# Kernel tuning notes

Measured on AMD Instinct MI355X. Metric: run time of the kernel, lower is better.

The kernel has to match this reference:

```python
import jax, jax.numpy as jnp
import numpy as np

N_NODES = 50000
N_EDGES = 800000
N_GRAPHS = 512
HEADS = 4
HDIM = 64
NEG_SLOPE = 0.2


def setup_inputs() -> dict:
    key = jax.random.key(0)
    ks = jax.random.split(key, 16)
    x = jax.random.normal(ks[0], (N_NODES, 128), dtype=jnp.float32)
    edge_index = jax.random.randint(ks[1], (2, N_EDGES), 0, N_NODES, dtype=jnp.int64)
    batch = jnp.sort(jax.random.randint(ks[2], (N_NODES,), 0, N_GRAPHS, dtype=jnp.int64))
    def glorot(k, shape):
        fan = shape[0] + shape[-1]
        return jax.random.normal(k, shape, dtype=jnp.float32) * jnp.sqrt(2.0 / fan)
    return {
        "x": x, "edge_index": edge_index, "batch": batch,
        "W1": glorot(ks[3], (128, 256)), "a_src1": glorot(ks[4], (HEADS, HDIM)), "a_dst1": glorot(ks[5], (HEADS, HDIM)), "b1": jnp.zeros((256,), jnp.float32),
        "W2": glorot(ks[6], (256, 256)), "a_src2": glorot(ks[7], (HEADS, HDIM)), "a_dst2": glorot(ks[8], (HEADS, HDIM)), "b2": jnp.zeros((256,), jnp.float32),
        "W3": glorot(ks[9], (256, 256)), "a_src3": glorot(ks[10], (HEADS, HDIM)), "a_dst3": glorot(ks[11], (HEADS, HDIM)), "b3": jnp.zeros((256,), jnp.float32),
        "fc_W": glorot(ks[12], (256, 1)), "fc_b": jnp.zeros((1,), jnp.float32),
    }


def gat_layer(x, W, a_src, a_dst, b, src, dst):
    # x: [N, F_in] -> h: [N, H, C]
    N = x.shape[0]
    h = (x @ W).reshape(N, HEADS, HDIM)
    alpha_s = jnp.sum(h * a_src[None], axis=-1)  # [N, H]
    alpha_d = jnp.sum(h * a_dst[None], axis=-1)  # [N, H]
    logits = jax.nn.leaky_relu(alpha_s[src] + alpha_d[dst], NEG_SLOPE)  # [E, H]
    # segment softmax over destination nodes
    m = jax.ops.segment_max(logits, dst, num_segments=N)  # [N, H]
    e = jnp.exp(logits - m[dst])
    denom = jax.ops.segment_sum(e, dst, num_segments=N)
    alpha = e / denom[dst]  # [E, H]
    msg = h[src] * alpha[:, :, None]  # [E, H, C]
    out = jax.ops.segment_sum(msg, dst, num_segments=N).reshape(N, HEADS * HDIM)
    return out + b


def reference(x, edge_index, batch, W1, a_src1, a_dst1, b1, W2, a_src2, a_dst2, b2, W3, a_src3, a_dst3, b3, fc_W, fc_b):
    N = x.shape[0]
    loop = jnp.arange(N, dtype=edge_index.dtype)
    # PyG GATConv adds self-loops by default
    src = jnp.concatenate([edge_index[0], loop])
    dst = jnp.concatenate([edge_index[1], loop])
    h = gat_layer(x, W1, a_src1, a_dst1, b1, src, dst)
    h = gat_layer(h, W2, a_src2, a_dst2, b2, src, dst)
    h = gat_layer(h, W3, a_src3, a_dst3, b3, src, dst)
    pooled = jax.ops.segment_sum(h, batch, num_segments=N_GRAPHS)  # [G, 256]
    return pooled @ fc_W + fc_b
```

## Files before the change

kernel.cpp:

```cpp
#include <hip/hip_runtime.h>
#include <hip/hip_bf16.h>
#include <math.h>

#define NN 50000
#define NE 800000
#define ET (NE + NN)
#define NG 512
#define NEG 0.2f

typedef __attribute__((ext_vector_type(8))) short bf16x8;
typedef __attribute__((ext_vector_type(4))) float f32x4;

__device__ inline unsigned f2o(float f) {
    unsigned b = __float_as_uint(f);
    return (b & 0x80000000u) ? ~b : (b | 0x80000000u);
}
__device__ inline float o2f(unsigned u) {
    return (u & 0x80000000u) ? __uint_as_float(u ^ 0x80000000u) : __uint_as_float(~u);
}
__device__ inline unsigned short f2b(float f) {
    unsigned u = __float_as_uint(f);
    u += 0x7fffu + ((u >> 16) & 1u);
    return (unsigned short)(u >> 16);
}
__device__ inline float b2f(unsigned short b) {
    return __uint_as_float(((unsigned)b) << 16);
}

__global__ __launch_bounds__(256) void split_weights(const float* __restrict__ W1,
        const float* __restrict__ W2, const float* __restrict__ W3,
        unsigned short* __restrict__ WTh, unsigned short* __restrict__ WTl) {
    int tid = blockIdx.x * 256 + threadIdx.x;
    const float* W; int K, n, k, base;
    if (tid < 32768)       { W = W1; K = 128; base = 0;     int i = tid;          n = i >> 7; k = i & 127; }
    else if (tid < 98304)  { W = W2; K = 256; base = 32768; int i = tid - 32768;  n = i >> 8; k = i & 255; }
    else if (tid < 163840) { W = W3; K = 256; base = 98304; int i = tid - 98304;  n = i >> 8; k = i & 255; }
    else return;
    float w = W[k * 256 + n];
    unsigned short hi = f2b(w);
    float lo = w - b2f(hi);
    WTh[base + n * K + k] = hi;
    WTl[base + n * K + k] = f2b(lo);
}

template<int K, int AFP32>
__global__ __launch_bounds__(256) void gemm_mfma(const float* __restrict__ Af,
        const unsigned short* __restrict__ Ahi, const unsigned short* __restrict__ Alo,
        const unsigned short* __restrict__ Bhi, const unsigned short* __restrict__ Blo,
        unsigned short* __restrict__ h,
        const float* __restrict__ a_src, const float* __restrict__ a_dst,
        float* __restrict__ as_, float* __restrict__ ad_,
        unsigned* __restrict__ gmax) {
    __shared__ unsigned short AsH[128][40], AsL[128][40], BsH[128][40], BsL[128][40];
    const int t = threadIdx.x;
    const int mb = blockIdx.x >> 1, nb = blockIdx.x & 1;
    const int m0 = mb * 128, n0 = nb * 128;
    const int wid = t >> 6, lane = t & 63;
    const int wr = wid >> 1, wc = wid & 1;
    const int lr = lane & 15, lg = lane >> 4;

    f32x4 acc[4][4];
    #pragma unroll
    for (int mi = 0; mi < 4; ++mi)
        #pragma unroll
        for (int ni = 0; ni < 4; ++ni)
            acc[mi][ni] = (f32x4){0.f, 0.f, 0.f, 0.f};

    for (int k0 = 0; k0 < K; k0 += 32) {
        __syncthreads();
        #pragma unroll
        for (int cc = 0; cc < 2; ++cc) {
            int c = t + cc * 256;
            int row = c >> 2, kc = c & 3;
            int gr = m0 + row; if (gr >= NN) gr = NN - 1;
            if (AFP32) {
                const float* pa = Af + (size_t)gr * K + k0 + kc * 8;
                float4 f0 = *(const float4*)pa;
                float4 f1 = *(const float4*)(pa + 4);
                union { unsigned short u[8]; uint4 v; } th, tl;
                float fs[8] = {f0.x, f0.y, f0.z, f0.w, f1.x, f1.y, f1.z, f1.w};
                #pragma unroll
                for (int j = 0; j < 8; ++j) {
                    unsigned short hv = f2b(fs[j]);
                    th.u[j] = hv;
                    tl.u[j] = f2b(fs[j] - b2f(hv));
                }
                *(uint4*)&AsH[row][kc * 8] = th.v;
                *(uint4*)&AsL[row][kc * 8] = tl.v;
            } else {
                *(uint4*)&AsH[row][kc * 8] = *(const uint4*)(Ahi + (size_t)gr * K + k0 + kc * 8);
                *(uint4*)&AsL[row][kc * 8] = *(const uint4*)(Alo + (size_t)gr * K + k0 + kc * 8);
            }
            *(uint4*)&BsH[row][kc * 8] = *(const uint4*)(Bhi + (size_t)(n0 + row) * K + k0 + kc * 8);
            *(uint4*)&BsL[row][kc * 8] = *(const uint4*)(Blo + (size_t)(n0 + row) * K + k0 + kc * 8);
        }
        __syncthreads();

        bf16x8 ah[4], al[4];
        #pragma unroll
        for (int mi = 0; mi < 4; ++mi) {
            int ra = wr * 64 + mi * 16 + lr;
            ah[mi] = *(const bf16x8*)&AsH[ra][lg * 8];
            al[mi] = *(const bf16x8*)&AsL[ra][lg * 8];
        }
        #pragma unroll
        for (int ni = 0; ni < 4; ++ni) {
            int rb = wc * 64 + ni * 16 + lr;
            bf16x8 bh = *(const bf16x8*)&BsH[rb][lg * 8];
            bf16x8 bl = *(const bf16x8*)&BsL[rb][lg * 8];
            #pragma unroll
            for (int mi = 0; mi < 4; ++mi) {
                acc[mi][ni] = __builtin_amdgcn_mfma_f32_16x16x32_bf16(bh, ah[mi], acc[mi][ni], 0, 0, 0);
                acc[mi][ni] = __builtin_amdgcn_mfma_f32_16x16x32_bf16(bh, al[mi], acc[mi][ni], 0, 0, 0);
                acc[mi][ni] = __builtin_amdgcn_mfma_f32_16x16x32_bf16(bl, ah[mi], acc[mi][ni], 0, 0, 0);
            }
        }
    }

    const int head = nb * 2 + wc;
    const int ncol0 = n0 + wc * 64;
    float4 asv[4], adv[4];
    #pragma unroll
    for (int ni = 0; ni < 4; ++ni) {
        asv[ni] = *(const float4*)&a_src[head * 64 + ni * 16 + lg * 4];
        adv[ni] = *(const float4*)&a_dst[head * 64 + ni * 16 + lg * 4];
    }
    float pmax = -1e30f;
    #pragma unroll
    for (int mi = 0; mi < 4; ++mi) {
        float ps = 0.f, pd = 0.f;
        #pragma unroll
        for (int ni = 0; ni < 4; ++ni) {
            ps = fmaf(acc[mi][ni][0], asv[ni].x, ps); pd = fmaf(acc[mi][ni][0], adv[ni].x, pd);
            ps = fmaf(acc[mi][ni][1], asv[ni].y, ps); pd = fmaf(acc[mi][ni][1], adv[ni].y, pd);
            ps = fmaf(acc[mi][ni][2], asv[ni].z, ps); pd = fmaf(acc[mi][ni][2], adv[ni].z, pd);
            ps = fmaf(acc[mi][ni][3], asv[ni].w, ps); pd = fmaf(acc[mi][ni][3], adv[ni].w, pd);
        }
        ps += __shfl_xor(ps, 16, 64); ps += __shfl_xor(ps, 32, 64);
        pd += __shfl_xor(pd, 16, 64); pd += __shfl_xor(pd, 32, 64);
        pmax = fmaxf(pmax, ps);
        int row = m0 + wr * 64 + mi * 16 + lr;
        if (row < NN) {
            #pragma unroll
            for (int ni = 0; ni < 4; ++ni) {
                ushort4 hv = {f2b(acc[mi][ni][0]), f2b(acc[mi][ni][1]),
                              f2b(acc[mi][ni][2]), f2b(acc[mi][ni][3])};
                *(ushort4*)&h[(size_t)row * 256 + ncol0 + ni * 16 + lg * 4] = hv;
            }
            if (lane < 16) { as_[row * 4 + head] = ps; ad_[row * 4 + head] = pd; }
        }
    }
    pmax = fmaxf(pmax, __shfl_xor(pmax, 1, 64));
    pmax = fmaxf(pmax, __shfl_xor(pmax, 2, 64));
    pmax = fmaxf(pmax, __shfl_xor(pmax, 4, 64));
    pmax = fmaxf(pmax, __shfl_xor(pmax, 8, 64));
    if (lane == 0) atomicMax(&gmax[head], f2o(pmax));
}

__global__ void init_counts(int* counts, int* esrc_pad, unsigned* gmax) {
    int i = blockIdx.x * 256 + threadIdx.x;
    if (i < NN) counts[i] = 1;
    if (i < 24) esrc_pad[i] = 0;
    if (i < 12) gmax[i] = 0u;
}
__global__ void count_kernel(const int* __restrict__ dst, int* counts) {
    int e = blockIdx.x * 256 + threadIdx.x;
    if (e < NE) atomicAdd(&counts[dst[e]], 1);
}
__global__ __launch_bounds__(1024) void scan_kernel(const int* __restrict__ counts,
                                                    int* row_ptr, int* cursor) {
    __shared__ int sm[1024];
    const int i = threadIdx.x;
    const int CH = (NN + 1023) / 1024;
    int base = i * CH;
    int s = 0;
    for (int j = 0; j < CH; ++j) { int idx = base + j; if (idx < NN) s += counts[idx]; }
    sm[i] = s; __syncthreads();
    for (int off = 1; off < 1024; off <<= 1) {
        int v = (i >= off) ? sm[i - off] : 0;
        __syncthreads();
        sm[i] += v;
        __syncthreads();
    }
    int run = sm[i] - s;
    for (int j = 0; j < CH; ++j) {
        int idx = base + j;
        if (idx < NN) { row_ptr[idx] = run; cursor[idx] = run; run += counts[idx]; }
    }
    if (i == 1023) row_ptr[NN] = ET;
}
__global__ void scatter_kernel(const int* __restrict__ src, const int* __restrict__ dst,
                               int* cursor, int* esrc) {
    int e = blockIdx.x * 256 + threadIdx.x;
    if (e < NE) {
        int p = atomicAdd(&cursor[dst[e]], 1);
        esrc[p] = src[e];
    } else if (e < ET) {
        int n = e - NE;
        int p = atomicAdd(&cursor[n], 1);
        esrc[p] = n;
    }
}

#define EDGE(ae, he)                                                           \
    {                                                                          \
        float t_ = (ae) + adn; t_ = t_ > 0.f ? t_ : NEG * t_;                  \
        float w_ = __expf(t_ - g); lsum += w_;                                 \
        acc.x = fmaf(w_, b2f((he).x), acc.x);                                  \
        acc.y = fmaf(w_, b2f((he).y), acc.y);                                  \
        acc.z = fmaf(w_, b2f((he).z), acc.z);                                  \
        acc.w = fmaf(w_, b2f((he).w), acc.w);                                  \
    }

template<int FINAL>
__global__ __launch_bounds__(256) void agg_kernel(const unsigned short* __restrict__ h,
        const float* __restrict__ as_, const float* __restrict__ ad_,
        const unsigned* __restrict__ gmax,
        const int* __restrict__ row_ptr, const int* __restrict__ esrc,
        const float* __restrict__ bias,
        unsigned short* __restrict__ ohi, unsigned short* __restrict__ olo,
        float* __restrict__ out,
        const int* __restrict__ batch, const float* __restrict__ fcW) {
    int n = blockIdx.x * 4 + (threadIdx.x >> 6);
    int lane = threadIdx.x & 63;
    if (n >= NN) return;
    const int head = lane >> 4;
    const int c4 = lane * 4;
    int s0 = row_ptr[n], s1 = row_ptr[n + 1];
    float adn = ad_[n * 4 + head];
    float g = o2f(gmax[head]) + adn; g = g > 0.f ? g : NEG * g;
    float lsum = 0.f;
    float4 acc = {0.f, 0.f, 0.f, 0.f};

    int i = s0;
    int iC[4], iD[4];
    float aA[4], aB[4]; ushort4 hA[4], hB[4];
    {
        int iA[4], iB[4];
        #pragma unroll
        for (int j = 0; j < 4; ++j) iA[j] = esrc[i + j];
        #pragma unroll
        for (int j = 0; j < 4; ++j) iB[j] = esrc[i + 4 + j];
        #pragma unroll
        for (int j = 0; j < 4; ++j) { aA[j] = as_[iA[j] * 4 + head]; hA[j] = *(const ushort4*)&h[(long)iA[j] * 256 + c4]; }
        #pragma unroll
        for (int j = 0; j < 4; ++j) { aB[j] = as_[iB[j] * 4 + head]; hB[j] = *(const ushort4*)&h[(long)iB[j] * 256 + c4]; }
        #pragma unroll
        for (int j = 0; j < 4; ++j) iC[j] = esrc[i + 8 + j];
        #pragma unroll
        for (int j = 0; j < 4; ++j) iD[j] = esrc[i + 12 + j];
    }

    while (i + 16 <= s1) {
        #pragma unroll
        for (int j = 0; j < 4; ++j) EDGE(aA[j], hA[j]);
        #pragma unroll
        for (int j = 0; j < 4; ++j) { aA[j] = as_[iC[j] * 4 + head]; hA[j] = *(const ushort4*)&h[(long)iC[j] * 256 + c4]; }
        #pragma unroll
        for (int j = 0; j < 4; ++j) iC[j] = esrc[i + 16 + j];
        #pragma unroll
        for (int j = 0; j < 4; ++j) EDGE(aB[j], hB[j]);
        #pragma unroll
        for (int j = 0; j < 4; ++j) { aB[j] = as_[iD[j] * 4 + head]; hB[j] = *(const ushort4*)&h[(long)iD[j] * 256 + c4]; }
        #pragma unroll
        for (int j = 0; j < 4; ++j) iD[j] = esrc[i + 20 + j];
        i += 8;
    }

    int r = s1 - i;
    if (r > 8) {
        #pragma unroll
        for (int j = 0; j < 4; ++j) EDGE(aA[j], hA[j]);
        #pragma unroll
        for (int j = 0; j < 4; ++j) EDGE(aB[j], hB[j]);
        #pragma unroll
        for (int j = 0; j < 4; ++j) { aA[j] = as_[iC[j] * 4 + head]; hA[j] = *(const ushort4*)&h[(long)iC[j] * 256 + c4]; }
        #pragma unroll
        for (int j = 0; j < 4; ++j) { aB[j] = as_[iD[j] * 4 + head]; hB[j] = *(const ushort4*)&h[(long)iD[j] * 256 + c4]; }
        r -= 8;
    }
    #pragma unroll
    for (int j = 0; j < 4; ++j) {
        float t_ = aA[j] + adn; t_ = t_ > 0.f ? t_ : NEG * t_;
        float w_ = (j < r) ? __expf(t_ - g) : 0.f;
        lsum += w_;
        acc.x = fmaf(w_, b2f(hA[j].x), acc.x);
        acc.y = fmaf(w_, b2f(hA[j].y), acc.y);
        acc.z = fmaf(w_, b2f(hA[j].z), acc.z);
        acc.w = fmaf(w_, b2f(hA[j].w), acc.w);
    }
    #pragma unroll
    for (int j = 0; j < 4; ++j) {
        float t_ = aB[j] + adn; t_ = t_ > 0.f ? t_ : NEG * t_;
        float w_ = (4 + j < r) ? __expf(t_ - g) : 0.f;
        lsum += w_;
        acc.x = fmaf(w_, b2f(hB[j].x), acc.x);
        acc.y = fmaf(w_, b2f(hB[j].y), acc.y);
        acc.z = fmaf(w_, b2f(hB[j].z), acc.z);
        acc.w = fmaf(w_, b2f(hB[j].w), acc.w);
    }

    float rl = 1.f / lsum;
    float4 bv = *(const float4*)&bias[c4];
    float4 o = {fmaf(acc.x, rl, bv.x), fmaf(acc.y, rl, bv.y),
                fmaf(acc.z, rl, bv.z), fmaf(acc.w, rl, bv.w)};
    if (!FINAL) {
        ushort4 vh = {f2b(o.x), f2b(o.y), f2b(o.z), f2b(o.w)};
        ushort4 vl = {f2b(o.x - b2f(vh.x)), f2b(o.y - b2f(vh.y)),
                      f2b(o.z - b2f(vh.z)), f2b(o.w - b2f(vh.w))};
        *(ushort4*)&ohi[(long)n * 256 + c4] = vh;
        *(ushort4*)&olo[(long)n * 256 + c4] = vl;
    } else {
        float4 fw = *(const float4*)&fcW[c4];
        float sd = o.x * fw.x + o.y * fw.y + o.z * fw.z + o.w * fw.w;
        #pragma unroll
        for (int off = 32; off; off >>= 1) sd += __shfl_xor(sd, off, 64);
        if (lane == 0) atomicAdd(&out[batch[n]], sd);
    }
}

__global__ void out_init(const float* __restrict__ fc_b, float* out) {
    int i = blockIdx.x * 256 + threadIdx.x;
    if (i < NG) out[i] = fc_b[0];
}

extern "C" void kernel_launch(void* const* d_in, const int* in_sizes, int n_in,
                              void* d_out, int out_size, void* d_ws, size_t ws_size,
                              hipStream_t stream) {
    const float* x      = (const float*)d_in[0];
    const int*   ei     = (const int*)d_in[1];
    const int*   batch  = (const int*)d_in[2];
    const float* W1     = (const float*)d_in[3];
    const float* as1    = (const float*)d_in[4];
    const float* ad1    = (const float*)d_in[5];
    const float* b1     = (const float*)d_in[6];
    const float* W2     = (const float*)d_in[7];
    const float* as2    = (const float*)d_in[8];
    const float* ad2    = (const float*)d_in[9];
    const float* b2     = (const float*)d_in[10];
    const float* W3     = (const float*)d_in[11];
    const float* as3    = (const float*)d_in[12];
    const float* ad3    = (const float*)d_in[13];
    const float* b3     = (const float*)d_in[14];
    const float* fcW    = (const float*)d_in[15];
    const float* fcb    = (const float*)d_in[16];
    const int* esrc_in = ei;
    const int* edst_in = ei + NE;

    char* ws = (char*)d_ws;
    size_t off = 0;
    unsigned short* hB  = (unsigned short*)(ws + off); off += (size_t)NN * 256 * 2;
    unsigned short* ohi = (unsigned short*)(ws + off); off += (size_t)NN * 256 * 2;
    unsigned short* olo = (unsigned short*)(ws + off); off += (size_t)NN * 256 * 2;
    unsigned short* WTh = (unsigned short*)(ws + off); off += 163840 * 2;
    unsigned short* WTl = (unsigned short*)(ws + off); off += 163840 * 2;
    float* aS    = (float*)(ws + off); off += (size_t)NN * 4 * 4;
    float* aD    = (float*)(ws + off); off += (size_t)NN * 4 * 4;
    int* counts  = (int*)(ws + off);   off += (size_t)NN * 4;
    int* cursor  = (int*)(ws + off);   off += (size_t)NN * 4;
    int* row_ptr = (int*)(ws + off);   off += (size_t)(NN + 1) * 4 + 12;
    unsigned* gmax = (unsigned*)(ws + off); off += 48;
    int* esrc    = (int*)(ws + off);   off += (size_t)(ET + 24) * 4;
    float* out   = (float*)d_out;

    init_counts<<<(NN + 255) / 256, 256, 0, stream>>>(counts, esrc + ET, gmax);
    count_kernel<<<(NE + 255) / 256, 256, 0, stream>>>(edst_in, counts);
    scan_kernel<<<1, 1024, 0, stream>>>(counts, row_ptr, cursor);
    scatter_kernel<<<(ET + 255) / 256, 256, 0, stream>>>(esrc_in, edst_in, cursor, esrc);
    split_weights<<<640, 256, 0, stream>>>(W1, W2, W3, WTh, WTl);

    const int GEMM_GRID = ((NN + 127) / 128) * 2;
    const int NODE_GRID = (NN + 3) / 4;

    gemm_mfma<128, 1><<<GEMM_GRID, 256, 0, stream>>>(x, nullptr, nullptr, WTh, WTl, hB, as1, ad1, aS, aD, gmax);
    agg_kernel<0><<<NODE_GRID, 256, 0, stream>>>(hB, aS, aD, gmax, row_ptr, esrc, b1, ohi, olo, nullptr, nullptr, nullptr);
    gemm_mfma<256, 0><<<GEMM_GRID, 256, 0, stream>>>(nullptr, ohi, olo, WTh + 32768, WTl + 32768, hB, as2, ad2, aS, aD, gmax + 4);
    agg_kernel<0><<<NODE_GRID, 256, 0, stream>>>(hB, aS, aD, gmax + 4, row_ptr, esrc, b2, ohi, olo, nullptr, nullptr, nullptr);
    gemm_mfma<256, 0><<<GEMM_GRID, 256, 0, stream>>>(nullptr, ohi, olo, WTh + 98304, WTl + 98304, hB, as3, ad3, aS, aD, gmax + 8);
    out_init<<<(NG + 255) / 256, 256, 0, stream>>>(fcb, out);
    agg_kernel<1><<<NODE_GRID, 256, 0, stream>>>(hB, aS, aD, gmax + 8, row_ptr, esrc, b3, nullptr, nullptr, out, batch, fcW);
}
```

Measured before the change: 668.1 us.

## Precompute per-edge softmax weights in a separate edge kernel before aggregation

Adds an edge_w kernel that computes exp(leaky_relu(aS[src]+aD[dst]) - bound) for every edge and head into a wE buffer. This needs a dst array built during the CSR scatter. The aggregation kernel then reads these weights instead of gathering aS per source and evaluating exp. Its software pipeline is also reshaped from a two-stage 16-edge prefetch to a one-stage 4-edge prefetch with a scalar tail. This removes the random aS gather and the exp work from the latency-bound aggregation loop. In exchange it adds three extra launches and roughly 13.6 MB of weight writes plus reads per layer, and the shallower prefetch may expose more gather latency.

```diff
diff --git a/kernel.cpp b/kernel.cpp
--- a/kernel.cpp
+++ b/kernel.cpp
@@ -5,6 +5,7 @@
 #define NN 50000
 #define NE 800000
 #define ET (NE + NN)
+#define EP (ET + 24)
 #define NG 512
 #define NEG 0.2f
 
@@ -157,10 +158,10 @@
     if (lane == 0) atomicMax(&gmax[head], f2o(pmax));
 }
 
-__global__ void init_counts(int* counts, int* esrc_pad, unsigned* gmax) {
+__global__ void init_counts(int* counts, int* esrc_pad, int* edst_pad, unsigned* gmax) {
     int i = blockIdx.x * 256 + threadIdx.x;
     if (i < NN) counts[i] = 1;
-    if (i < 24) esrc_pad[i] = 0;
+    if (i < 24) { esrc_pad[i] = 0; edst_pad[i] = 0; }
     if (i < 12) gmax[i] = 0u;
 }
 __global__ void count_kernel(const int* __restrict__ dst, int* counts) {
@@ -190,32 +191,48 @@
     if (i == 1023) row_ptr[NN] = ET;
 }
 __global__ void scatter_kernel(const int* __restrict__ src, const int* __restrict__ dst,
-                               int* cursor, int* esrc) {
+                               int* cursor, int* esrc, int* edst) {
     int e = blockIdx.x * 256 + threadIdx.x;
     if (e < NE) {
-        int p = atomicAdd(&cursor[dst[e]], 1);
+        int d = dst[e];
+        int p = atomicAdd(&cursor[d], 1);
         esrc[p] = src[e];
+        edst[p] = d;
     } else if (e < ET) {
         int n = e - NE;
         int p = atomicAdd(&cursor[n], 1);
         esrc[p] = n;
-    }
-}
-
-#define EDGE(ae, he)                                                           \
+        edst[p] = n;
+    }
+}
+
+__global__ __launch_bounds__(256) void edge_w(const int* __restrict__ esrc,
+        const int* __restrict__ edst, const float* __restrict__ aS,
+        const float* __restrict__ aD, const unsigned* __restrict__ gmax,
+        float* __restrict__ wE) {
+    int idx = blockIdx.x * 256 + threadIdx.x;
+    if (idx >= EP * 4) return;
+    int e = idx >> 2, hd = idx & 3;
+    if (e >= ET) { wE[idx] = 0.f; return; }
+    int s = esrc[e], d = edst[e];
+    float adn = aD[d * 4 + hd];
+    float t = aS[s * 4 + hd] + adn; t = t > 0.f ? t : NEG * t;
+    float g = o2f(gmax[hd]) + adn;  g = g > 0.f ? g : NEG * g;
+    wE[idx] = __expf(t - g);
+}
+
+#define EDGE(we, he)                                                           \
     {                                                                          \
-        float t_ = (ae) + adn; t_ = t_ > 0.f ? t_ : NEG * t_;                  \
-        float w_ = __expf(t_ - g); lsum += w_;                                 \
-        acc.x = fmaf(w_, b2f((he).x), acc.x);                                  \
-        acc.y = fmaf(w_, b2f((he).y), acc.y);                                  \
-        acc.z = fmaf(w_, b2f((he).z), acc.z);                                  \
-        acc.w = fmaf(w_, b2f((he).w), acc.w);                                  \
+        lsum += (we);                                                          \
+        acc.x = fmaf((we), b2f((he).x), acc.x);                                \
+        acc.y = fmaf((we), b2f((he).y), acc.y);                                \
+        acc.z = fmaf((we), b2f((he).z), acc.z);                                \
+        acc.w = fmaf((we), b2f((he).w), acc.w);                                \
     }
 
 template<int FINAL>
 __global__ __launch_bounds__(256) void agg_kernel(const unsigned short* __restrict__ h,
-        const float* __restrict__ as_, const float* __restrict__ ad_,
-        const unsigned* __restrict__ gmax,
+        const float* __restrict__ wE,
         const int* __restrict__ row_ptr, const int* __restrict__ esrc,
         const float* __restrict__ bias,
         unsigned short* __restrict__ ohi, unsigned short* __restrict__ olo,
@@ -227,77 +244,45 @@
     const int head = lane >> 4;
     const int c4 = lane * 4;
     int s0 = row_ptr[n], s1 = row_ptr[n + 1];
-    float adn = ad_[n * 4 + head];
-    float g = o2f(gmax[head]) + adn; g = g > 0.f ? g : NEG * g;
     float lsum = 0.f;
     float4 acc = {0.f, 0.f, 0.f, 0.f};
 
     int i = s0;
-    int iC[4], iD[4];
-    float aA[4], aB[4]; ushort4 hA[4], hB[4];
-    {
-        int iA[4], iB[4];
-        #pragma unroll
-        for (int j = 0; j < 4; ++j) iA[j] = esrc[i + j];
-        #pragma unroll
-        for (int j = 0; j < 4; ++j) iB[j] = esrc[i + 4 + j];
-        #pragma unroll
-        for (int j = 0; j < 4; ++j) { aA[j] = as_[iA[j] * 4 + head]; hA[j] = *(const ushort4*)&h[(long)iA[j] * 256 + c4]; }
-        #pragma unroll
-        for (int j = 0; j < 4; ++j) { aB[j] = as_[iB[j] * 4 + head]; hB[j] = *(const ushort4*)&h[(long)iB[j] * 256 + c4]; }
+    int iA[4], iB[4];
+    float wA[4]; ushort4 hA[4];
+    #pragma unroll
+    for (int j = 0; j < 4; ++j) iA[j] = esrc[i + j];
+    #pragma unroll
+    for (int j = 0; j < 4; ++j) iB[j] = esrc[i + 4 + j];
+    #pragma unroll
+    for (int j = 0; j < 4; ++j) wA[j] = wE[(i + j) * 4 + head];
+    #pragma unroll
+    for (int j = 0; j < 4; ++j) hA[j] = *(const ushort4*)&h[(long)iA[j] * 256 + c4];
+
+    while (i + 8 <= s1) {
+        int iC[4];
         #pragma unroll
         for (int j = 0; j < 4; ++j) iC[j] = esrc[i + 8 + j];
-        #pragma unroll
-        for (int j = 0; j < 4; ++j) iD[j] = esrc[i + 12 + j];
-    }
-
-    while (i + 16 <= s1) {
-        #pragma unroll
-        for (int j = 0; j < 4; ++j) EDGE(aA[j], hA[j]);
-        #pragma unroll
-        for (int j = 0; j < 4; ++j) { aA[j] = as_[iC[j] * 4 + head]; hA[j] = *(const ushort4*)&h[(long)iC[j] * 256 + c4]; }
-        #pragma unroll
-        for (int j = 0; j < 4; ++j) iC[j] = esrc[i + 16 + j];
-        #pragma unroll
-        for (int j = 0; j < 4; ++j) EDGE(aB[j], hB[j]);
-        #pragma unroll
-        for (int j = 0; j < 4; ++j) { aB[j] = as_[iD[j] * 4 + head]; hB[j] = *(const ushort4*)&h[(long)iD[j] * 256 + c4]; }
-        #pragma unroll
-        for (int j = 0; j < 4; ++j) iD[j] = esrc[i + 20 + j];
-        i += 8;
-    }
-
-    int r = s1 - i;
-    if (r > 8) {
-        #pragma unroll
-        for (int j = 0; j < 4; ++j) EDGE(aA[j], hA[j]);
-        #pragma unroll
-        for (int j = 0; j < 4; ++j) EDGE(aB[j], hB[j]);
-        #pragma unroll
-        for (int j = 0; j < 4; ++j) { aA[j] = as_[iC[j] * 4 + head]; hA[j] = *(const ushort4*)&h[(long)iC[j] * 256 + c4]; }
-        #pragma unroll
-        for (int j = 0; j < 4; ++j) { aB[j] = as_[iD[j] * 4 + head]; hB[j] = *(const ushort4*)&h[(long)iD[j] * 256 + c4]; }
-        r -= 8;
-    }
-    #pragma unroll
-    for (int j = 0; j < 4; ++j) {
-        float t_ = aA[j] + adn; t_ = t_ > 0.f ? t_ : NEG * t_;
-        float w_ = (j < r) ? __expf(t_ - g) : 0.f;
-        lsum += w_;
-        acc.x = fmaf(w_, b2f(hA[j].x), acc.x);
-        acc.y = fmaf(w_, b2f(hA[j].y), acc.y);
-        acc.z = fmaf(w_, b2f(hA[j].z), acc.z);
-        acc.w = fmaf(w_, b2f(hA[j].w), acc.w);
-    }
-    #pragma unroll
-    for (int j = 0; j < 4; ++j) {
-        float t_ = aB[j] + adn; t_ = t_ > 0.f ? t_ : NEG * t_;
-        float w_ = (4 + j < r) ? __expf(t_ - g) : 0.f;
-        lsum += w_;
-        acc.x = fmaf(w_, b2f(hB[j].x), acc.x);
-        acc.y = fmaf(w_, b2f(hB[j].y), acc.y);
-        acc.z = fmaf(w_, b2f(hB[j].z), acc.z);
-        acc.w = fmaf(w_, b2f(hB[j].w), acc.w);
+        float wB[4]; ushort4 hB[4];
+        #pragma unroll
+        for (int j = 0; j < 4; ++j) wB[j] = wE[(i + 4 + j) * 4 + head];
+        #pragma unroll
+        for (int j = 0; j < 4; ++j) hB[j] = *(const ushort4*)&h[(long)iB[j] * 256 + c4];
+        #pragma unroll
+        for (int j = 0; j < 4; ++j) EDGE(wA[j], hA[j]);
+        #pragma unroll
+        for (int j = 0; j < 4; ++j) { iB[j] = iC[j]; wA[j] = wB[j]; hA[j] = hB[j]; }
+        i += 4;
+    }
+    if (i + 4 <= s1) {
+        #pragma unroll
+        for (int j = 0; j < 4; ++j) EDGE(wA[j], hA[j]);
+        i += 4;
+    }
+    for (; i < s1; ++i) {
+        float w = wE[i * 4 + head];
+        ushort4 hv = *(const ushort4*)&h[(long)esrc[i] * 256 + c4];
+        EDGE(w, hv);
     }
 
     float rl = 1.f / lsum;
@@ -360,23 +345,29 @@
     int* cursor  = (int*)(ws + off);   off += (size_t)NN * 4;
     int* row_ptr = (int*)(ws + off);   off += (size_t)(NN + 1) * 4 + 12;
     unsigned* gmax = (unsigned*)(ws + off); off += 48;
-    int* esrc    = (int*)(ws + off);   off += (size_t)(ET + 24) * 4;
+    int* esrc    = (int*)(ws + off);   off += (size_t)EP * 4;
+    int* edst    = (int*)(ws + off);   off += (size_t)EP * 4;
+    float* wE    = (float*)(ws + off); off += (size_t)EP * 4 * 4;
     float* out   = (float*)d_out;
 
-    init_counts<<<(NN + 255) / 256, 256, 0, stream>>>(counts, esrc + ET, gmax);
+    init_counts<<<(NN + 255) / 256, 256, 0, stream>>>(counts, esrc + ET, edst + ET, gmax);
     count_kernel<<<(NE + 255) / 256, 256, 0, stream>>>(edst_in, counts);
     scan_kernel<<<1, 1024, 0, stream>>>(counts, row_ptr, cursor);
-    scatter_kernel<<<(ET + 255) / 256, 256, 0, stream>>>(esrc_in, edst_in, cursor, esrc);
+    scatter_kernel<<<(ET + 255) / 256, 256, 0, stream>>>(esrc_in, edst_in, cursor, esrc, edst);
     split_weights<<<640, 256, 0, stream>>>(W1, W2, W3, WTh, WTl);
 
     const int GEMM_GRID = ((NN + 127) / 128) * 2;
     const int NODE_GRID = (NN + 3) / 4;
+    const int EW_GRID   = (EP * 4 + 255) / 256;
 
     gemm_mfma<128, 1><<<GEMM_GRID, 256, 0, stream>>>(x, nullptr, nullptr, WTh, WTl, hB, as1, ad1, aS, aD, gmax);
-    agg_kernel<0><<<NODE_GRID, 256, 0, stream>>>(hB, aS, aD, gmax, row_ptr, esrc, b1, ohi, olo, nullptr, nullptr, nullptr);
+    edge_w<<<EW_GRID, 256, 0, stream>>>(esrc, edst, aS, aD, gmax, wE);
+    agg_kernel<0><<<NODE_GRID, 256, 0, stream>>>(hB, wE, row_ptr, esrc, b1, ohi, olo, nullptr, nullptr, nullptr);
     gemm_mfma<256, 0><<<GEMM_GRID, 256, 0, stream>>>(nullptr, ohi, olo, WTh + 32768, WTl + 32768, hB, as2, ad2, aS, aD, gmax + 4);
-    agg_kernel<0><<<NODE_GRID, 256, 0, stream>>>(hB, aS, aD, gmax + 4, row_ptr, esrc, b2, ohi, olo, nullptr, nullptr, nullptr);
+    edge_w<<<EW_GRID, 256, 0, stream>>>(esrc, edst, aS, aD, gmax + 4, wE);
+    agg_kernel<0><<<NODE_GRID, 256, 0, stream>>>(hB, wE, row_ptr, esrc, b2, ohi, olo, nullptr, nullptr, nullptr);
     gemm_mfma<256, 0><<<GEMM_GRID, 256, 0, stream>>>(nullptr, ohi, olo, WTh + 98304, WTl + 98304, hB, as3, ad3, aS, aD, gmax + 8);
+    edge_w<<<EW_GRID, 256, 0, stream>>>(esrc, edst, aS, aD, gmax + 8, wE);
     out_init<<<(NG + 255) / 256, 256, 0, stream>>>(fcb, out);
-    agg_kernel<1><<<NODE_GRID, 256, 0, stream>>>(hB, aS, aD, gmax + 8, row_ptr, esrc, b3, nullptr, nullptr, out, batch, fcW);
-}
+    agg_kernel<1><<<NODE_GRID, 256, 0, stream>>>(hB, wE, row_ptr, esrc, b3, nullptr, nullptr, out, batch, fcW);
+}
```

Result: no change. 681.2 us (+2.0%).
